# Kernel optimization log

Hardware: AMD Instinct MI355X
Metric: run time of the kernel (lower is better)

Reference implementation:

```python
import jax, jax.numpy as jnp
import numpy as np

H, W = 32, 32
S = H * W            # 1024 tokens
B = 16
C = 256              # in_channels == out_channels
HEAD_DIM = 32
N_HEADS = C // HEAD_DIM      # 8
DIM = N_HEADS * HEAD_DIM     # 256
SCALE = DIM ** (-0.5)        # NOTE: full dim, as in the source


def _relative_position_index(h, w):
    # Faithful port of get_relative_position_index (numpy, static)
    coords = np.stack(np.meshgrid(np.arange(h), np.arange(w), indexing='ij'))  # [2,h,w]
    coords_flat = coords.reshape(2, -1)                                        # [2,S]
    rel = coords_flat[:, :, None] - coords_flat[:, None, :]                    # [2,S,S]
    rel = rel.transpose(1, 2, 0).copy()                                        # [S,S,2]
    rel[:, :, 0] += h - 1
    rel[:, :, 1] += w - 1
    rel[:, :, 0] *= 2 * w - 1
    return rel.sum(-1).reshape(-1).astype(np.int32)                            # [S*S]


def setup_inputs() -> dict:
    key = jax.random.key(0)
    ks = jax.random.split(key, 6)
    x = jax.random.normal(ks[0], (B, S, C), dtype=jnp.float32)
    w_qkv = jax.random.normal(ks[1], (3 * DIM, C), dtype=jnp.float32) * 0.02
    b_qkv = jnp.zeros((3 * DIM,), dtype=jnp.float32)
    w_merge = jax.random.normal(ks[2], (C, DIM), dtype=jnp.float32) * 0.02
    b_merge = jnp.zeros((C,), dtype=jnp.float32)
    rel_table = jax.random.normal(ks[3], ((2 * H - 1) * (2 * W - 1), N_HEADS), dtype=jnp.float32) * 0.02
    rel_index = jnp.asarray(_relative_position_index(H, W))  # [S*S] int32
    return {"x": x, "w_qkv": w_qkv, "b_qkv": b_qkv,
            "w_merge": w_merge, "b_merge": b_merge,
            "rel_table": rel_table, "rel_index": rel_index}


def reference(x, w_qkv, b_qkv, w_merge, b_merge, rel_table, rel_index):
    b = x.shape[0]
    qkv = x @ w_qkv.T + b_qkv                       # [B,S,3*DIM]
    q, k, v = jnp.split(qkv, 3, axis=-1)
    def heads(t):
        return t.reshape(b, S, N_HEADS, HEAD_DIM).transpose(0, 2, 1, 3)  # [B,H,S,D]
    q, k, v = heads(q), heads(k), heads(v)
    score = jnp.einsum('bhqd,bhkd->bhqk', q, k) * SCALE   # [B,H,S,S]
    # Faithful to source: torch.gather with index [S*S,1] reads column 0 only
    pos_bias = rel_table[rel_index, 0].reshape(1, 1, S, S)
    attn = jax.nn.softmax(score + pos_bias, axis=-1)
    out = jnp.einsum('bhqk,bhkd->bqhd', attn, v).reshape(b, S, DIM)
    return out @ w_merge.T + b_merge                # [B,S,C]
```

## Files before the change

### kernel.cpp

```cpp
#include <hip/hip_runtime.h>


typedef __attribute__((ext_vector_type(8))) short bf16x8;
typedef __attribute__((ext_vector_type(4))) float f32x4;

#define INV_LN2 1.44269504088896340736f

__device__ __forceinline__ unsigned short f2bf(float f) {
  union { float f; unsigned u; } v; v.f = f;
  unsigned r = v.u + 0x7fffu + ((v.u >> 16) & 1u);
  return (unsigned short)(r >> 16);
}
__device__ __forceinline__ float bf2f(unsigned short h) {
  union { unsigned u; float f; } v; v.u = ((unsigned)h) << 16;
  return v.f;
}

__global__ __launch_bounds__(256) void prep_kernel(
    const float* __restrict__ x, const float* __restrict__ wq,
    const float* __restrict__ wm, const float* __restrict__ tab,
    const int* __restrict__ idx,
    unsigned short* __restrict__ xb, unsigned short* __restrict__ wqb,
    unsigned short* __restrict__ wmb, unsigned short* __restrict__ biasb) {
  const long NX = 1048576, NW1 = 49152, NW2 = 16384, NB = 262144;
  long u = (long)blockIdx.x * 256 + threadIdx.x;
  if (u < NX) {
    float4 v = ((const float4*)x)[u];
    ushort4 o; o.x = f2bf(v.x); o.y = f2bf(v.y); o.z = f2bf(v.z); o.w = f2bf(v.w);
    ((ushort4*)xb)[u] = o;
  } else if (u < NX + NW1) {
    long t = u - NX;
    float4 v = ((const float4*)wq)[t];
    ushort4 o; o.x = f2bf(v.x); o.y = f2bf(v.y); o.z = f2bf(v.z); o.w = f2bf(v.w);
    ((ushort4*)wqb)[t] = o;
  } else if (u < NX + NW1 + NW2) {
    long t = u - NX - NW1;
    float4 v = ((const float4*)wm)[t];
    ushort4 o; o.x = f2bf(v.x); o.y = f2bf(v.y); o.z = f2bf(v.z); o.w = f2bf(v.w);
    ((ushort4*)wmb)[t] = o;
  } else if (u < NX + NW1 + NW2 + NB) {
    long t = u - NX - NW1 - NW2;
    int4 iv = ((const int4*)idx)[t];
    ushort4 o;
    o.x = f2bf(tab[(long)iv.x * 8] * INV_LN2);
    o.y = f2bf(tab[(long)iv.y * 8] * INV_LN2);
    o.z = f2bf(tab[(long)iv.z * 8] * INV_LN2);
    o.w = f2bf(tab[(long)iv.w * 8] * INV_LN2);
    ((ushort4*)biasb)[t] = o;
  }
}

template <int MODE>
__global__ __launch_bounds__(256) void gemm_k(
    const unsigned short* __restrict__ A, const unsigned short* __restrict__ Bw,
    const float* __restrict__ bias,
    unsigned short* __restrict__ q_ws, unsigned short* __restrict__ k_ws,
    unsigned short* __restrict__ v_ws, float* __restrict__ out) {
  __shared__ __align__(16) unsigned short As[128 * 40];
  __shared__ __align__(16) unsigned short Bs[128 * 40];
  const int tid = threadIdx.x;
  const int lane = tid & 63, wid = tid >> 6;
  const int wm = wid >> 1, wn = wid & 1;
  const int li = lane & 15, g = lane >> 4;
  const int m0 = blockIdx.y * 128;
  const int n0 = blockIdx.x * 128;
  f32x4 acc[4][4] = {};
  const int srow = tid >> 2, sg = tid & 3;
  const unsigned short* Ag = A + (long)(m0 + srow) * 256 + sg * 8;
  const unsigned short* Bg = Bw + (long)(n0 + srow) * 256 + sg * 8;

  for (int kt = 0; kt < 8; ++kt) {
    const int k0 = kt * 32;
    bf16x8 a0 = *(const bf16x8*)(Ag + k0);
    bf16x8 a1 = *(const bf16x8*)(Ag + 64 * 256 + k0);
    bf16x8 b0 = *(const bf16x8*)(Bg + k0);
    bf16x8 b1 = *(const bf16x8*)(Bg + 64 * 256 + k0);
    __syncthreads();
    *(bf16x8*)(As + srow * 40 + sg * 8) = a0;
    *(bf16x8*)(As + (srow + 64) * 40 + sg * 8) = a1;
    *(bf16x8*)(Bs + srow * 40 + sg * 8) = b0;
    *(bf16x8*)(Bs + (srow + 64) * 40 + sg * 8) = b1;
    __syncthreads();
    bf16x8 af[4], bfr[4];
#pragma unroll
    for (int mi = 0; mi < 4; mi++)
      af[mi] = *(const bf16x8*)(As + (wm * 64 + mi * 16 + li) * 40 + g * 8);
#pragma unroll
    for (int ni = 0; ni < 4; ni++)
      bfr[ni] = *(const bf16x8*)(Bs + (wn * 64 + ni * 16 + li) * 40 + g * 8);
#pragma unroll
    for (int mi = 0; mi < 4; mi++)
#pragma unroll
      for (int ni = 0; ni < 4; ni++)
        acc[mi][ni] = __builtin_amdgcn_mfma_f32_16x16x32_bf16(af[mi], bfr[ni], acc[mi][ni], 0, 0, 0);
  }

  if (MODE == 0) {
    const int sec = n0 >> 8;
    unsigned short* dst = (sec == 0) ? q_ws : ((sec == 1) ? k_ws : v_ws);
    const float qscale = 0.0625f * INV_LN2;
#pragma unroll
    for (int mi = 0; mi < 4; mi++)
#pragma unroll
      for (int ni = 0; ni < 4; ni++)
#pragma unroll
        for (int i = 0; i < 4; i++) {
          int m = m0 + wm * 64 + mi * 16 + g * 4 + i;
          int n = n0 + wn * 64 + ni * 16 + li;
          float val = acc[mi][ni][i] + bias[n];
          if (sec == 0) val *= qscale;
          int h = (n >> 5) & 7, d = n & 31;
          int b = m >> 10, s = m & 1023;
          dst[((long)(b * 8 + h) * 1024 + s) * 32 + d] = f2bf(val);
        }
  } else {
#pragma unroll
    for (int mi = 0; mi < 4; mi++)
#pragma unroll
      for (int ni = 0; ni < 4; ni++)
#pragma unroll
        for (int i = 0; i < 4; i++) {
          int m = m0 + wm * 64 + mi * 16 + g * 4 + i;
          int n = n0 + wn * 64 + ni * 16 + li;
          out[(long)m * 256 + n] = acc[mi][ni][i] + bias[n];
        }
  }
}

__global__ __launch_bounds__(256) void vtrans_kernel(
    const unsigned short* __restrict__ v, unsigned short* __restrict__ vt) {
  long u = (long)blockIdx.x * 256 + threadIdx.x;
  if (u >= 524288) return;
  int tok_lin = (int)(u >> 2);
  int dchunk = ((int)u & 3) * 8;
  int bh = tok_lin >> 10, s = tok_lin & 1023;
  bf16x8 r = *(const bf16x8*)(v + (long)tok_lin * 32 + dchunk);
  unsigned short* base = vt + (long)bh * 32768 + s;
#pragma unroll
  for (int j = 0; j < 8; j++) base[(long)(dchunk + j) * 1024] = (unsigned short)r[j];
}

__global__ __launch_bounds__(256) void attn_kernel(
    const unsigned short* __restrict__ q_ws, const unsigned short* __restrict__ k_ws,
    const unsigned short* __restrict__ vt_ws, const unsigned short* __restrict__ biasb,
    unsigned short* __restrict__ attno) {
  __shared__ __align__(16) unsigned short Ks[64 * 40];
  __shared__ __align__(16) unsigned short Vt[32 * 72];
  __shared__ __align__(16) unsigned short Bi[64 * 72];
  __shared__ __align__(16) unsigned short Ps[4][16 * 72];
  const int tid = threadIdx.x;
  const int lane = tid & 63, wid = tid >> 6;
  const int li = lane & 15, g = lane >> 4;
  const int bh = blockIdx.y;
  const int qblk = blockIdx.x * 64;
  const int q0 = qblk + wid * 16;
  const unsigned short* qb = q_ws + (long)bh * 32768;
  const unsigned short* kb = k_ws + (long)bh * 32768;
  const unsigned short* vb = vt_ws + (long)bh * 32768;

  bf16x8 qf = *(const bf16x8*)(qb + (q0 + li) * 32 + g * 8);

  bf16x8 onesf = {};
  if (li == 0) {
#pragma unroll
    for (int j = 0; j < 8; j++) onesf[j] = (short)0x3F80;
  }

  f32x4 o0 = {}, o1 = {}, o2 = {};
  const int kt = tid >> 2, kd = (tid & 3) * 8;
  const int vd = tid >> 3, vs = (tid & 7) * 8;
  const int bq = tid >> 2, bt = (tid & 3) * 16;
  unsigned short* Pw = Ps[wid];

  for (int kv0 = 0; kv0 < 1024; kv0 += 64) {
    bf16x8 kv8 = *(const bf16x8*)(kb + (kv0 + kt) * 32 + kd);
    bf16x8 vv8 = *(const bf16x8*)(vb + vd * 1024 + kv0 + vs);
    bf16x8 bb0 = *(const bf16x8*)(biasb + (long)(qblk + bq) * 1024 + kv0 + bt);
    bf16x8 bb1 = *(const bf16x8*)(biasb + (long)(qblk + bq) * 1024 + kv0 + bt + 8);
    __syncthreads();
    *(bf16x8*)(Ks + kt * 40 + kd) = kv8;
    *(bf16x8*)(Vt + vd * 72 + vs) = vv8;
    *(bf16x8*)(Bi + bq * 72 + bt) = bb0;
    *(bf16x8*)(Bi + bq * 72 + bt + 8) = bb1;
    __syncthreads();

    f32x4 sc[4];
#pragma unroll
    for (int c = 0; c < 4; c++) {
      const unsigned short* brow = Bi + (wid * 16 + g * 4) * 72 + c * 16 + li;
      f32x4 ci;
      ci[0] = bf2f(brow[0]);
      ci[1] = bf2f(brow[72]);
      ci[2] = bf2f(brow[144]);
      ci[3] = bf2f(brow[216]);
      bf16x8 kf = *(const bf16x8*)(Ks + (c * 16 + li) * 40 + g * 8);
      sc[c] = __builtin_amdgcn_mfma_f32_16x16x32_bf16(qf, kf, ci, 0, 0, 0);
    }

#pragma unroll
    for (int c = 0; c < 4; c++) {
      float p0 = exp2f(sc[c][0]);
      float p1 = exp2f(sc[c][1]);
      float p2 = exp2f(sc[c][2]);
      float p3 = exp2f(sc[c][3]);
      unsigned r01, r23;
      asm("v_cvt_pk_bf16_f32 %0, %1, %2" : "=v"(r01) : "v"(p0), "v"(p1));
      asm("v_cvt_pk_bf16_f32 %0, %1, %2" : "=v"(r23) : "v"(p2), "v"(p3));
      unsigned short* pb = Pw + (g * 4) * 72 + c * 16 + li;
      pb[0]   = (unsigned short)(r01 & 0xffffu);
      pb[72]  = (unsigned short)(r01 >> 16);
      pb[144] = (unsigned short)(r23 & 0xffffu);
      pb[216] = (unsigned short)(r23 >> 16);
    }

#pragma unroll
    for (int c2 = 0; c2 < 2; c2++) {
      bf16x8 pa  = *(const bf16x8*)(Pw + li * 72 + c2 * 32 + g * 8);
      bf16x8 vf0 = *(const bf16x8*)(Vt + li * 72 + c2 * 32 + g * 8);
      bf16x8 vf1 = *(const bf16x8*)(Vt + (li + 16) * 72 + c2 * 32 + g * 8);
      o0 = __builtin_amdgcn_mfma_f32_16x16x32_bf16(pa, vf0, o0, 0, 0, 0);
      o1 = __builtin_amdgcn_mfma_f32_16x16x32_bf16(pa, vf1, o1, 0, 0, 0);
      o2 = __builtin_amdgcn_mfma_f32_16x16x32_bf16(pa, onesf, o2, 0, 0, 0);
    }
  }

  const int b = bh >> 3, h = bh & 7;
#pragma unroll
  for (int i = 0; i < 4; i++) {
    float s = __shfl(o2[i], lane & 48, 64);
    float inv = 1.0f / s;
    int srow = q0 + g * 4 + i;
    long base = ((long)(b * 1024 + srow)) * 256 + h * 32;
    attno[base + li] = f2bf(o0[i] * inv);
    attno[base + 16 + li] = f2bf(o1[i] * inv);
  }
}

extern "C" void kernel_launch(void* const* d_in, const int* in_sizes, int n_in,
                              void* d_out, int out_size, void* d_ws, size_t ws_size,
                              hipStream_t stream) {
  const float* x      = (const float*)d_in[0];
  const float* wqkv   = (const float*)d_in[1];
  const float* bqkv   = (const float*)d_in[2];
  const float* wmerge = (const float*)d_in[3];
  const float* bmerge = (const float*)d_in[4];
  const float* rtab   = (const float*)d_in[5];
  const int*   ridx   = (const int*)d_in[6];
  float* out = (float*)d_out;

  char* ws = (char*)d_ws;
  unsigned short* xb    = (unsigned short*)(ws);
  unsigned short* wqb   = (unsigned short*)(ws + 8388608);
  unsigned short* wmb   = (unsigned short*)(ws + 8781824);
  unsigned short* biasb = (unsigned short*)(ws + 8912896);
  unsigned short* q_ws  = (unsigned short*)(ws + 11010048);
  unsigned short* k_ws  = (unsigned short*)(ws + 19398656);
  unsigned short* v_ws  = (unsigned short*)(ws + 27787264);
  unsigned short* attno = (unsigned short*)(ws + 36175872);
  unsigned short* vt_ws = xb;

  prep_kernel<<<5376, 256, 0, stream>>>(x, wqkv, wmerge, rtab, ridx, xb, wqb, wmb, biasb);
  gemm_k<0><<<dim3(6, 128), 256, 0, stream>>>(xb, wqb, bqkv, q_ws, k_ws, v_ws, nullptr);
  vtrans_kernel<<<2048, 256, 0, stream>>>(v_ws, vt_ws);
  attn_kernel<<<dim3(16, 128), 256, 0, stream>>>(q_ws, k_ws, vt_ws, biasb, attno);
  gemm_k<1><<<dim3(2, 128), 256, 0, stream>>>(attno, wmb, bmerge, nullptr, nullptr, nullptr, out);
}
```

Measured before the change: 117.4 us.

## Fuse V transpose into QKV GEMM epilogue and load bias directly in attention

The QKV GEMM epilogue now writes V directly in transposed [bh][d][s] layout, which removes the separate vtrans kernel and its launch plus extra memory pass. In the attention kernel, the score MFMA operands are swapped so each lane holds contiguous key positions. The positional bias is then read straight from global memory as packed uint2 instead of being staged through shared memory, and P is stored to LDS with one vector write per lane. exp2f is replaced by the hardware exp2 builtin. The transposed V stores in the GEMM epilogue are strided and may be less coalesced, and the bias reads now hit global/L2 per wave instead of being shared through LDS.

```diff
diff --git a/kernel.cpp b/kernel.cpp
--- a/kernel.cpp
+++ b/kernel.cpp
@@ -11,8 +11,8 @@
   unsigned r = v.u + 0x7fffu + ((v.u >> 16) & 1u);
   return (unsigned short)(r >> 16);
 }
-__device__ __forceinline__ float bf2f(unsigned short h) {
-  union { unsigned u; float f; } v; v.u = ((unsigned)h) << 16;
+__device__ __forceinline__ float u2f(unsigned u) {
+  union { unsigned u; float f; } v; v.u = u;
   return v.f;
 }
 
@@ -97,7 +97,7 @@
 
   if (MODE == 0) {
     const int sec = n0 >> 8;
-    unsigned short* dst = (sec == 0) ? q_ws : ((sec == 1) ? k_ws : v_ws);
+    unsigned short* dst = (sec == 0) ? q_ws : k_ws;
     const float qscale = 0.0625f * INV_LN2;
 #pragma unroll
     for (int mi = 0; mi < 4; mi++)
@@ -111,7 +111,10 @@
           if (sec == 0) val *= qscale;
           int h = (n >> 5) & 7, d = n & 31;
           int b = m >> 10, s = m & 1023;
-          dst[((long)(b * 8 + h) * 1024 + s) * 32 + d] = f2bf(val);
+          if (sec == 2)
+            v_ws[(long)(b * 8 + h) * 32768 + (long)d * 1024 + s] = f2bf(val);
+          else
+            dst[((long)(b * 8 + h) * 1024 + s) * 32 + d] = f2bf(val);
         }
   } else {
 #pragma unroll
@@ -125,19 +128,6 @@
           out[(long)m * 256 + n] = acc[mi][ni][i] + bias[n];
         }
   }
-}
-
-__global__ __launch_bounds__(256) void vtrans_kernel(
-    const unsigned short* __restrict__ v, unsigned short* __restrict__ vt) {
-  long u = (long)blockIdx.x * 256 + threadIdx.x;
-  if (u >= 524288) return;
-  int tok_lin = (int)(u >> 2);
-  int dchunk = ((int)u & 3) * 8;
-  int bh = tok_lin >> 10, s = tok_lin & 1023;
-  bf16x8 r = *(const bf16x8*)(v + (long)tok_lin * 32 + dchunk);
-  unsigned short* base = vt + (long)bh * 32768 + s;
-#pragma unroll
-  for (int j = 0; j < 8; j++) base[(long)(dchunk + j) * 1024] = (unsigned short)r[j];
 }
 
 __global__ __launch_bounds__(256) void attn_kernel(
@@ -146,7 +136,6 @@
     unsigned short* __restrict__ attno) {
   __shared__ __align__(16) unsigned short Ks[64 * 40];
   __shared__ __align__(16) unsigned short Vt[32 * 72];
-  __shared__ __align__(16) unsigned short Bi[64 * 72];
   __shared__ __align__(16) unsigned short Ps[4][16 * 72];
   const int tid = threadIdx.x;
   const int lane = tid & 63, wid = tid >> 6;
@@ -157,6 +146,7 @@
   const unsigned short* qb = q_ws + (long)bh * 32768;
   const unsigned short* kb = k_ws + (long)bh * 32768;
   const unsigned short* vb = vt_ws + (long)bh * 32768;
+  const unsigned short* bias_row = biasb + (long)(q0 + li) * 1024;
 
   bf16x8 qf = *(const bf16x8*)(qb + (q0 + li) * 32 + g * 8);
 
@@ -169,48 +159,40 @@
   f32x4 o0 = {}, o1 = {}, o2 = {};
   const int kt = tid >> 2, kd = (tid & 3) * 8;
   const int vd = tid >> 3, vs = (tid & 7) * 8;
-  const int bq = tid >> 2, bt = (tid & 3) * 16;
   unsigned short* Pw = Ps[wid];
 
   for (int kv0 = 0; kv0 < 1024; kv0 += 64) {
     bf16x8 kv8 = *(const bf16x8*)(kb + (kv0 + kt) * 32 + kd);
     bf16x8 vv8 = *(const bf16x8*)(vb + vd * 1024 + kv0 + vs);
-    bf16x8 bb0 = *(const bf16x8*)(biasb + (long)(qblk + bq) * 1024 + kv0 + bt);
-    bf16x8 bb1 = *(const bf16x8*)(biasb + (long)(qblk + bq) * 1024 + kv0 + bt + 8);
     __syncthreads();
     *(bf16x8*)(Ks + kt * 40 + kd) = kv8;
     *(bf16x8*)(Vt + vd * 72 + vs) = vv8;
-    *(bf16x8*)(Bi + bq * 72 + bt) = bb0;
-    *(bf16x8*)(Bi + bq * 72 + bt + 8) = bb1;
     __syncthreads();
 
     f32x4 sc[4];
 #pragma unroll
     for (int c = 0; c < 4; c++) {
-      const unsigned short* brow = Bi + (wid * 16 + g * 4) * 72 + c * 16 + li;
+      uint2 bd = *(const uint2*)(bias_row + kv0 + c * 16 + g * 4);
       f32x4 ci;
-      ci[0] = bf2f(brow[0]);
-      ci[1] = bf2f(brow[72]);
-      ci[2] = bf2f(brow[144]);
-      ci[3] = bf2f(brow[216]);
+      ci[0] = u2f(bd.x << 16);
+      ci[1] = u2f(bd.x & 0xffff0000u);
+      ci[2] = u2f(bd.y << 16);
+      ci[3] = u2f(bd.y & 0xffff0000u);
       bf16x8 kf = *(const bf16x8*)(Ks + (c * 16 + li) * 40 + g * 8);
-      sc[c] = __builtin_amdgcn_mfma_f32_16x16x32_bf16(qf, kf, ci, 0, 0, 0);
+      sc[c] = __builtin_amdgcn_mfma_f32_16x16x32_bf16(kf, qf, ci, 0, 0, 0);
     }
 
 #pragma unroll
     for (int c = 0; c < 4; c++) {
-      float p0 = exp2f(sc[c][0]);
-      float p1 = exp2f(sc[c][1]);
-      float p2 = exp2f(sc[c][2]);
-      float p3 = exp2f(sc[c][3]);
+      float p0 = __builtin_amdgcn_exp2f(sc[c][0]);
+      float p1 = __builtin_amdgcn_exp2f(sc[c][1]);
+      float p2 = __builtin_amdgcn_exp2f(sc[c][2]);
+      float p3 = __builtin_amdgcn_exp2f(sc[c][3]);
       unsigned r01, r23;
       asm("v_cvt_pk_bf16_f32 %0, %1, %2" : "=v"(r01) : "v"(p0), "v"(p1));
       asm("v_cvt_pk_bf16_f32 %0, %1, %2" : "=v"(r23) : "v"(p2), "v"(p3));
-      unsigned short* pb = Pw + (g * 4) * 72 + c * 16 + li;
-      pb[0]   = (unsigned short)(r01 & 0xffffu);
-      pb[72]  = (unsigned short)(r01 >> 16);
-      pb[144] = (unsigned short)(r23 & 0xffffu);
-      pb[216] = (unsigned short)(r23 >> 16);
+      uint2 pk; pk.x = r01; pk.y = r23;
+      *(uint2*)(Pw + li * 72 + c * 16 + g * 4) = pk;
     }
 
 #pragma unroll
@@ -257,11 +239,9 @@
   unsigned short* k_ws  = (unsigned short*)(ws + 19398656);
   unsigned short* v_ws  = (unsigned short*)(ws + 27787264);
   unsigned short* attno = (unsigned short*)(ws + 36175872);
-  unsigned short* vt_ws = xb;
 
   prep_kernel<<<5376, 256, 0, stream>>>(x, wqkv, wmerge, rtab, ridx, xb, wqb, wmb, biasb);
   gemm_k<0><<<dim3(6, 128), 256, 0, stream>>>(xb, wqb, bqkv, q_ws, k_ws, v_ws, nullptr);
-  vtrans_kernel<<<2048, 256, 0, stream>>>(v_ws, vt_ws);
-  attn_kernel<<<dim3(16, 128), 256, 0, stream>>>(q_ws, k_ws, vt_ws, biasb, attno);
+  attn_kernel<<<dim3(16, 128), 256, 0, stream>>>(q_ws, k_ws, v_ws, biasb, attno);
   gemm_k<1><<<dim3(2, 128), 256, 0, stream>>>(attno, wmb, bmerge, nullptr, nullptr, nullptr, out);
 }
```

After: 114.3 us. 1.03x faster.
